# Optimization experiments

Measured on AMD Instinct MI355X. Metric: run time of the kernel, lower is better.

Reference implementation:

```python
import jax, jax.numpy as jnp
import numpy as np

B, C, H, W = 4, 256, 64, 64
RC = 32  # reduced channels = C // reduction


def setup_inputs() -> dict:
    key = jax.random.key(0)
    ks = jax.random.split(key, 5)
    return {
        "x": jax.random.normal(ks[0], (B, C, H, W), dtype=jnp.float32),
        "context": jax.random.normal(ks[1], (B, C, H, W), dtype=jnp.float32),
        "Wq": jax.random.normal(ks[2], (RC, C), dtype=jnp.float32) * 0.02,
        "bq": jnp.zeros((RC,), dtype=jnp.float32),
        "Wk": jax.random.normal(ks[3], (RC, C), dtype=jnp.float32) * 0.02,
        "bk": jnp.zeros((RC,), dtype=jnp.float32),
        "Wv": jax.random.normal(ks[4], (C, C), dtype=jnp.float32) * 0.02,
        "bv": jnp.zeros((C,), dtype=jnp.float32),
        "gamma": jnp.ones((1,), dtype=jnp.float32),
    }


def reference(x, context, Wq, bq, Wk, bk, Wv, bv, gamma):
    b, c, h, w = x.shape
    _, _, hc, wc = context.shape
    n, m = h * w, hc * wc
    xf = x.reshape(b, c, n)          # (B,C,N)
    cf = context.reshape(b, c, m)    # (B,C,M)
    # 1x1 conv projections == per-pixel linear
    q = jnp.einsum('rc,bcn->bnr', Wq, xf) + bq            # (B,N,RC)
    k = jnp.einsum('rc,bcm->brm', Wk, cf) + bk[:, None]   # (B,RC,M)
    v = jnp.einsum('dc,bcm->bdm', Wv, cf) + bv[:, None]   # (B,C,M)
    scale = 1.0 / jnp.sqrt(jnp.asarray(q.shape[-1], dtype=q.dtype))
    attn = jax.nn.softmax(jnp.einsum('bnr,brm->bnm', q, k) * scale, axis=-1)  # (B,N,M)
    out = jnp.einsum('bdm,bnm->bdn', v, attn).reshape(b, c, h, w)
    return gamma * out + x
```

## Files before the change

### kernel.cpp

```cpp
#include <hip/hip_runtime.h>
#include <hip/hip_bf16.h>


#define B_ 4
#define C_ 256
#define N_ 4096
#define M_ 4096
#define SCALE2_ 0.25509558269734695f

typedef __bf16 bf16x8 __attribute__((ext_vector_type(8)));
typedef float f32x4 __attribute__((ext_vector_type(4)));
typedef float f32x16 __attribute__((ext_vector_type(16)));
typedef int i32x8 __attribute__((ext_vector_type(8)));

#define AS1 __attribute__((address_space(1)))
#define AS3 __attribute__((address_space(3)))

static __device__ __forceinline__ unsigned short f2bf(float f) {
    unsigned int u = __float_as_uint(f);
    return (unsigned short)((u + 0x7fffu + ((u >> 16) & 1u)) >> 16);
}
static __device__ __forceinline__ unsigned bfpk(float a, float b) {
    return (unsigned)f2bf(a) | ((unsigned)f2bf(b) << 16);
}
static __device__ __forceinline__ void p_barrier() {
    asm volatile("s_waitcnt lgkmcnt(0)" ::: "memory");
    __builtin_amdgcn_s_barrier();
    asm volatile("" ::: "memory");
}

__global__ __launch_bounds__(256) void prep(
        const float* __restrict__ Wq, const float* __restrict__ Wk,
        const float* __restrict__ Wv, uint4* __restrict__ Wqf,
        uint4* __restrict__ Wkf, uint4* __restrict__ Wvf) {
    int bid = blockIdx.x, t = threadIdx.x;
    const float* W;
    uint4* dst;
    int frag;
    if (bid < 32)      { W = Wv; dst = Wvf; frag = (bid * 256 + t) >> 6; }
    else if (bid < 36) { W = Wq; dst = Wqf; frag = ((bid - 32) * 256 + t) >> 6; }
    else               { W = Wk; dst = Wkf; frag = ((bid - 36) * 256 + t) >> 6; }
    int lane = t & 63, low = lane & 15, q = lane >> 4;
    int fch = frag & 7, fr = frag >> 3;
    const float* wp = W + (size_t)(fr * 16 + low) * C_ + fch * 32 + q * 8;
    float4 w0 = *(const float4*)wp;
    float4 w1 = *(const float4*)(wp + 4);
    uint4 pk = {bfpk(w0.x, w0.y), bfpk(w0.z, w0.w),
                bfpk(w1.x, w1.y), bfpk(w1.z, w1.w)};
    dst[(size_t)frag * 64 + lane] = pk;
}

__global__ __launch_bounds__(256, 2) void fused_proj(
        const float* __restrict__ x, const float* __restrict__ ctx,
        const uint4* __restrict__ Wqf, const uint4* __restrict__ Wkf,
        const uint4* __restrict__ Wvf,
        const float* __restrict__ bq, const float* __restrict__ bk,
        const float* __restrict__ bv,
        unsigned short* __restrict__ Qf, unsigned short* __restrict__ Kf,
        unsigned char* __restrict__ Vf) {
    __shared__ unsigned short X[64][264];
    __shared__ unsigned short Pl[4][16 * 40];
    __shared__ unsigned char  Vw[4][16 * 40];

    int bid = blockIdx.x;
    bool isX = bid >= 256;
    int lb = bid & 255;
    int b = lb >> 6, pt64 = lb & 63;
    const float* __restrict__ in = (isX ? x : ctx) + (size_t)b * C_ * N_ + pt64 * 64;
    int t = threadIdx.x, wg = t >> 6, lane = t & 63;
    int low = lane & 15, q = lane >> 4;

    {
        int pL = lane;
        const float* s0 = in + pL;
#pragma unroll
        for (int ct = 0; ct < 4; ct++) {
            const float* s2 = s0 + (size_t)(ct * 64 + wg * 16) * N_;
            float v[16];
#pragma unroll
            for (int k = 0; k < 16; k++) v[k] = s2[(size_t)k * N_];
#pragma unroll
            for (int k = 0; k < 16; k += 2)
                *(unsigned*)&X[pL][ct * 64 + wg * 16 + k] = bfpk(v[k], v[k + 1]);
        }
    }
    __syncthreads();

    {
        const uint4* __restrict__ Wf = isX ? Wqf : Wkf;
        const float* __restrict__ bias = isX ? bq : bk;
        unsigned short* __restrict__ dst = isX ? Qf : Kf;
        bf16x8 xf[8];
#pragma unroll
        for (int ch = 0; ch < 8; ch++)
            xf[ch] = *(const bf16x8*)&X[wg * 16 + low][ch * 32 + q * 8];
        const f32x4 zero = {0.f, 0.f, 0.f, 0.f};
        f32x4 acc[2] = {zero, zero};
#pragma unroll
        for (int rt = 0; rt < 2; rt++)
#pragma unroll
            for (int ch = 0; ch < 8; ch++) {
                uint4 wv = Wf[(rt * 8 + ch) * 64 + lane];
                acc[rt] = __builtin_amdgcn_mfma_f32_16x16x32_bf16(
                    __builtin_bit_cast(bf16x8, wv), xf[ch], acc[rt], 0, 0, 0);
            }
        unsigned short* Pw = &Pl[wg][0];
#pragma unroll
        for (int rt = 0; rt < 2; rt++) {
            float b0 = bias[rt * 16 + q * 4 + 0], b1 = bias[rt * 16 + q * 4 + 1];
            float b2 = bias[rt * 16 + q * 4 + 2], b3 = bias[rt * 16 + q * 4 + 3];
            uint2 pk = {bfpk(acc[rt][0] + b0, acc[rt][1] + b1),
                        bfpk(acc[rt][2] + b2, acc[rt][3] + b3)};
            *(uint2*)(Pw + low * 40 + rt * 16 + q * 4) = pk;
        }
        uint4 frag = *(const uint4*)(Pw + low * 40 + q * 8);
        ((uint4*)dst)[((size_t)b * 256 + pt64 * 4 + wg) * 64 + lane] = frag;
    }

    if (!isX) {
        int mstep = wg >> 1, dh = wg & 1;
        bf16x8 vfr[2][8];
#pragma unroll
        for (int mt = 0; mt < 2; mt++)
#pragma unroll
            for (int ch = 0; ch < 8; ch++)
                vfr[mt][ch] = *(const bf16x8*)&X[mstep * 32 + mt * 16 + low][ch * 32 + q * 8];
        unsigned char* Vv = &Vw[wg][0];
        int msg = pt64 * 2 + mstep;
        const f32x4 zero = {0.f, 0.f, 0.f, 0.f};
#pragma unroll
        for (int dt8 = 0; dt8 < 8; dt8++) {
            int dt = dh * 8 + dt8;
            f32x4 a0 = zero, a1 = zero;
#pragma unroll
            for (int ch = 0; ch < 8; ch++) {
                uint4 wv = Wvf[(dt * 8 + ch) * 64 + lane];
                bf16x8 wfr = __builtin_bit_cast(bf16x8, wv);
                a0 = __builtin_amdgcn_mfma_f32_16x16x32_bf16(vfr[0][ch], wfr, a0, 0, 0, 0);
                a1 = __builtin_amdgcn_mfma_f32_16x16x32_bf16(vfr[1][ch], wfr, a1, 0, 0, 0);
            }
            float bb = bv[dt * 16 + low];
            unsigned w0 = __builtin_amdgcn_cvt_pk_fp8_f32(a0[0] + bb, a0[1] + bb, 0, false);
            w0 = __builtin_amdgcn_cvt_pk_fp8_f32(a0[2] + bb, a0[3] + bb, w0, true);
            unsigned w1 = __builtin_amdgcn_cvt_pk_fp8_f32(a1[0] + bb, a1[1] + bb, 0, false);
            w1 = __builtin_amdgcn_cvt_pk_fp8_f32(a1[2] + bb, a1[3] + bb, w1, true);
            *(unsigned*)(Vv + low * 40 + q * 4) = w0;
            *(unsigned*)(Vv + low * 40 + 16 + q * 4) = w1;
            uint2 fr = *(const uint2*)(Vv + low * 40 + q * 8);
            ((uint2*)Vf)[(((size_t)b * 128 + msg) * 16 + dt) * 64 + lane] = fr;
        }
    }
}

__global__ __launch_bounds__(256, 4) void attn(
        const unsigned short* __restrict__ Qf, const unsigned short* __restrict__ Kf,
        const unsigned char* __restrict__ Vf, const float* __restrict__ x,
        const float* __restrict__ gamma, float* __restrict__ out) {
    __shared__ __align__(16) unsigned char Pb[2][2560];
    __shared__ float l_sh[2][32];
    __shared__ unsigned Ot[32 * 129];

    int bid = blockIdx.x;
    int xcd = bid & 7;
    int b = xcd >> 1;
    int ng = ((xcd & 1) << 6) | (bid >> 3);

    int wg = threadIdx.x >> 6, lane = threadIdx.x & 63;
    int q = lane >> 4, low = lane & 15;
    int hi = lane >> 5;
    int dsel = q & 1;
    int l31 = lane & 31;
    int t = wg & 1;
    int h = wg >> 1;

    const uint4* Qp = (const uint4*)Qf;
    const uint4* Kp = (const uint4*)Kf + (size_t)b * 256 * 64;
    const uint2* Vq = (const uint2*)(Vf + (size_t)b * 1048576) + (size_t)hi * 1024 + low;

    bf16x8 qa = __builtin_bit_cast(bf16x8, Qp[(size_t)(b * 256 + ng * 2 + t) * 64 + lane]);

    f32x16 acc2[2];
    acc2[0] = (f32x16)(0.f);
    acc2[1] = (f32x16)(0.f);
    float lacc = 0.f;
    const f32x4 zero = {0.f, 0.f, 0.f, 0.f};

    uint4 kv[2];
    f32x4 s[2];
    {
#pragma unroll
        for (int u = 0; u < 2; u++)
            kv[u] = Kp[(size_t)(h * 2 + u) * 64 + lane];
#pragma unroll
        for (int u = 0; u < 2; u++)
            s[u] = __builtin_amdgcn_mfma_f32_16x16x32_bf16(
                __builtin_bit_cast(bf16x8, kv[u]), qa, zero, 0, 0, 0);
#pragma unroll
        for (int u = 0; u < 2; u++)
            kv[u] = Kp[(size_t)(4 + h * 2 + u) * 64 + lane];
        unsigned char* Pw = &Pb[0][0];
#pragma unroll
        for (int u = 0; u < 2; u++) {
            float p0 = __builtin_amdgcn_exp2f(s[u][0] * SCALE2_);
            float p1 = __builtin_amdgcn_exp2f(s[u][1] * SCALE2_);
            float p2 = __builtin_amdgcn_exp2f(s[u][2] * SCALE2_);
            float p3 = __builtin_amdgcn_exp2f(s[u][3] * SCALE2_);
            lacc += p0 + p1 + p2 + p3;
            unsigned w = __builtin_amdgcn_cvt_pk_fp8_f32(p0, p1, 0, false);
            w = __builtin_amdgcn_cvt_pk_fp8_f32(p2, p3, w, true);
            *(unsigned*)(Pw + t * 1280 + low * 80 + h * 32 + u * 16 + q * 4) = w;
        }
    }
    i32x8 vf[2];
#pragma unroll
    for (int dg = 0; dg < 2; dg++) {
        int dt = wg * 4 + dg * 2 + dsel;
        const uint2* Vs = Vq + dt * 64;
        long* dqw = (long*)&vf[dg];
#pragma unroll
        for (int ss = 0; ss < 4; ss++)
            dqw[ss] = *(const long*)(Vs + ss * 16);
    }
    p_barrier();

    for (int i = 0; i < 64; i++) {
        int cur = i & 1, nxt = cur ^ 1;
        bool hn = (i + 1 < 64);

        if (hn) {
#pragma unroll
            for (int u = 0; u < 2; u++)
                s[u] = __builtin_amdgcn_mfma_f32_16x16x32_bf16(
                    __builtin_bit_cast(bf16x8, kv[u]), qa, zero, 0, 0, 0);
            if (i + 2 < 64) {
#pragma unroll
                for (int u = 0; u < 2; u++)
                    kv[u] = Kp[(size_t)((i + 2) * 4 + h * 2 + u) * 64 + lane];
            }
        }

        {
            const unsigned char* pr = &Pb[cur][0] + dsel * 1280 + low * 80 + hi * 32;
            i32x8 pf;
            ((uint4*)&pf)[0] = *(const uint4*)pr;
            ((uint4*)&pf)[1] = *(const uint4*)(pr + 16);
#pragma unroll
            for (int dg = 0; dg < 2; dg++)
                acc2[dg] = __builtin_amdgcn_mfma_scale_f32_32x32x64_f8f6f4(
                    vf[dg], pf, acc2[dg], 0, 0, 0, 127, 0, 127);
        }

        if (hn) {
#pragma unroll
            for (int dg = 0; dg < 2; dg++) {
                int dt = wg * 4 + dg * 2 + dsel;
                const uint2* Vs = Vq + (size_t)(i + 1) * 2048 + dt * 64;
                long* dqw = (long*)&vf[dg];
#pragma unroll
                for (int ss = 0; ss < 4; ss++)
                    dqw[ss] = *(const long*)(Vs + ss * 16);
            }
        }

        if (hn) {
            unsigned char* Pw = &Pb[nxt][0];
#pragma unroll
            for (int u = 0; u < 2; u++) {
                float p0 = __builtin_amdgcn_exp2f(s[u][0] * SCALE2_);
                float p1 = __builtin_amdgcn_exp2f(s[u][1] * SCALE2_);
                float p2 = __builtin_amdgcn_exp2f(s[u][2] * SCALE2_);
                float p3 = __builtin_amdgcn_exp2f(s[u][3] * SCALE2_);
                lacc += p0 + p1 + p2 + p3;
                unsigned w = __builtin_amdgcn_cvt_pk_fp8_f32(p0, p1, 0, false);
                w = __builtin_amdgcn_cvt_pk_fp8_f32(p2, p3, w, true);
                *(unsigned*)(Pw + t * 1280 + low * 80 + h * 32 + u * 16 + q * 4) = w;
            }
        }
        p_barrier();
    }

    lacc += __shfl_xor(lacc, 16, 64);
    lacc += __shfl_xor(lacc, 32, 64);
    if (lane < 16)
        l_sh[h][t * 16 + low] = lacc;

#pragma unroll
    for (int dg = 0; dg < 2; dg++)
#pragma unroll
        for (int k = 0; k < 8; k++) {
            int col16 = wg * 32 + dg * 16 + (k & 1) + 4 * (k >> 1) + 2 * hi;
            Ot[l31 * 129 + col16] = bfpk(acc2[dg][2 * k], acc2[dg][2 * k + 1]);
        }
    __syncthreads();

    {
        float gm = gamma[0];
        float rinv = gm / (l_sh[0][l31] + l_sh[1][l31]);
        int dh = hi;
#pragma unroll
        for (int dq = 0; dq < 2; dq++) {
            size_t nb = ((size_t)(b * 256 + wg * 64 + dq * 32 + dh * 16)) * 4096
                        + (size_t)ng * 32 + l31;
#pragma unroll 4
            for (int j = 0; j < 16; j++) {
                unsigned pk = Ot[l31 * 129 + wg * 32 + dq * 16 + dh * 8 + (j >> 1)];
                unsigned bits = (j & 1) ? (pk & 0xffff0000u) : (pk << 16);
                float o = __uint_as_float(bits);
                size_t idx = nb + (size_t)j * 4096;
                out[idx] = o * rinv + x[idx];
            }
        }
    }
}

extern "C" void kernel_launch(void* const* d_in, const int* in_sizes, int n_in,
                              void* d_out, int out_size, void* d_ws, size_t ws_size,
                              hipStream_t stream) {
    const float* x     = (const float*)d_in[0];
    const float* ctx   = (const float*)d_in[1];
    const float* Wq    = (const float*)d_in[2];
    const float* bq    = (const float*)d_in[3];
    const float* Wk    = (const float*)d_in[4];
    const float* bk    = (const float*)d_in[5];
    const float* Wv    = (const float*)d_in[6];
    const float* bv    = (const float*)d_in[7];
    const float* gamma = (const float*)d_in[8];
    float* out = (float*)d_out;

    unsigned short* Qf = (unsigned short*)d_ws;
    unsigned short* Kf = Qf + (size_t)B_ * N_ * 32;
    unsigned char*  Vf = (unsigned char*)(Kf + (size_t)B_ * M_ * 32);
    uint4* Wqf = (uint4*)(Vf + (size_t)B_ * M_ * C_);
    uint4* Wkf = Wqf + 16 * 64;
    uint4* Wvf = Wkf + 16 * 64;

    prep<<<40, 256, 0, stream>>>(Wq, Wk, Wv, Wqf, Wkf, Wvf);
    fused_proj<<<512, 256, 0, stream>>>(x, ctx, Wqf, Wkf, Wvf, bq, bk, bv, Qf, Kf, Vf);
    attn<<<512, 256, 0, stream>>>(Qf, Kf, Vf, x, gamma, out);
}
```

Measured before the change: 145.0 us.

## Restructure attention to 16-query blocks with 16x16x128 fp8 MFMA and row-major V

Attention blocks now each handle 16 queries instead of 32, so the grid doubles to 1024 blocks. Each wave owns a 64-channel slice of V and loops over 128-key chunks using 16x16x128 scaled fp8 MFMAs instead of 32x32x64. The projection kernel writes V in a plain channel-major transposed layout, and the LDS staging of the output is dropped, so results are written directly from the accumulators. V fragments are prefetched one iteration ahead, and exp2 with a pre-folded scale is replaced by __expf. The aim is more parallelism and a simpler epilogue, at the cost of reloading Q and K per smaller block and less coalesced V stores.

```diff
diff --git a/kernel.cpp b/kernel.cpp
--- a/kernel.cpp
+++ b/kernel.cpp
@@ -6,11 +6,10 @@
 #define C_ 256
 #define N_ 4096
 #define M_ 4096
-#define SCALE2_ 0.25509558269734695f
+#define SCALE_ 0.17677669529663687f
 
 typedef __bf16 bf16x8 __attribute__((ext_vector_type(8)));
 typedef float f32x4 __attribute__((ext_vector_type(4)));
-typedef float f32x16 __attribute__((ext_vector_type(16)));
 typedef int i32x8 __attribute__((ext_vector_type(8)));
 
 #define AS1 __attribute__((address_space(1)))
@@ -57,10 +56,9 @@
         const float* __restrict__ bq, const float* __restrict__ bk,
         const float* __restrict__ bv,
         unsigned short* __restrict__ Qf, unsigned short* __restrict__ Kf,
-        unsigned char* __restrict__ Vf) {
+        unsigned char* __restrict__ Vt) {
     __shared__ unsigned short X[64][264];
     __shared__ unsigned short Pl[4][16 * 40];
-    __shared__ unsigned char  Vw[4][16 * 40];
 
     int bid = blockIdx.x;
     bool isX = bid >= 256;
@@ -125,7 +123,6 @@
 #pragma unroll
             for (int ch = 0; ch < 8; ch++)
                 vfr[mt][ch] = *(const bf16x8*)&X[mstep * 32 + mt * 16 + low][ch * 32 + q * 8];
-        unsigned char* Vv = &Vw[wg][0];
         int msg = pt64 * 2 + mstep;
         const f32x4 zero = {0.f, 0.f, 0.f, 0.f};
 #pragma unroll
@@ -144,137 +141,120 @@
             w0 = __builtin_amdgcn_cvt_pk_fp8_f32(a0[2] + bb, a0[3] + bb, w0, true);
             unsigned w1 = __builtin_amdgcn_cvt_pk_fp8_f32(a1[0] + bb, a1[1] + bb, 0, false);
             w1 = __builtin_amdgcn_cvt_pk_fp8_f32(a1[2] + bb, a1[3] + bb, w1, true);
-            *(unsigned*)(Vv + low * 40 + q * 4) = w0;
-            *(unsigned*)(Vv + low * 40 + 16 + q * 4) = w1;
-            uint2 fr = *(const uint2*)(Vv + low * 40 + q * 8);
-            ((uint2*)Vf)[(((size_t)b * 128 + msg) * 16 + dt) * 64 + lane] = fr;
+            unsigned* vr = (unsigned*)(Vt + ((size_t)(b * 256 + dt * 16 + low)) * 4096
+                                          + msg * 32 + q * 4);
+            vr[0] = w0;
+            vr[4] = w1;
         }
     }
 }
 
 __global__ __launch_bounds__(256, 4) void attn(
         const unsigned short* __restrict__ Qf, const unsigned short* __restrict__ Kf,
-        const unsigned char* __restrict__ Vf, const float* __restrict__ x,
+        const unsigned char* __restrict__ Vt, const float* __restrict__ x,
         const float* __restrict__ gamma, float* __restrict__ out) {
-    __shared__ __align__(16) unsigned char Pb[2][2560];
-    __shared__ float l_sh[2][32];
-    __shared__ unsigned Ot[32 * 129];
+    __shared__ __align__(16) unsigned char Pb[2][64 * 136];
+    __shared__ float l_sh[4][16];
 
     int bid = blockIdx.x;
-    int xcd = bid & 7;
+    int xcd = bid & 7, cu5 = (bid >> 3) & 31, qs = bid >> 8;
     int b = xcd >> 1;
-    int ng = ((xcd & 1) << 6) | (bid >> 3);
+    int g = ((((xcd & 1) << 5) | cu5) << 2) | qs;
 
     int wg = threadIdx.x >> 6, lane = threadIdx.x & 63;
     int q = lane >> 4, low = lane & 15;
-    int hi = lane >> 5;
-    int dsel = q & 1;
-    int l31 = lane & 31;
-    int t = wg & 1;
-    int h = wg >> 1;
 
     const uint4* Qp = (const uint4*)Qf;
     const uint4* Kp = (const uint4*)Kf + (size_t)b * 256 * 64;
-    const uint2* Vq = (const uint2*)(Vf + (size_t)b * 1048576) + (size_t)hi * 1024 + low;
-
-    bf16x8 qa = __builtin_bit_cast(bf16x8, Qp[(size_t)(b * 256 + ng * 2 + t) * 64 + lane]);
-
-    f32x16 acc2[2];
-    acc2[0] = (f32x16)(0.f);
-    acc2[1] = (f32x16)(0.f);
+    const unsigned char* Vrow = Vt + ((size_t)(b * 256 + wg * 64 + low)) * 4096 + q * 32;
+
+    bf16x8 qa = __builtin_bit_cast(bf16x8, Qp[(size_t)(b * 256 + g) * 64 + lane]);
+
+    f32x4 acc[4];
+#pragma unroll
+    for (int dd = 0; dd < 4; dd++) acc[dd] = (f32x4){0.f, 0.f, 0.f, 0.f};
     float lacc = 0.f;
     const f32x4 zero = {0.f, 0.f, 0.f, 0.f};
 
     uint4 kv[2];
     f32x4 s[2];
+#pragma unroll
+    for (int u = 0; u < 2; u++)
+        kv[u] = Kp[(size_t)(wg * 2 + u) * 64 + lane];
+#pragma unroll
+    for (int u = 0; u < 2; u++)
+        s[u] = __builtin_amdgcn_mfma_f32_16x16x32_bf16(
+            __builtin_bit_cast(bf16x8, kv[u]), qa, zero, 0, 0, 0);
+#pragma unroll
+    for (int u = 0; u < 2; u++)
+        kv[u] = Kp[(size_t)(8 + wg * 2 + u) * 64 + lane];
     {
-#pragma unroll
-        for (int u = 0; u < 2; u++)
-            kv[u] = Kp[(size_t)(h * 2 + u) * 64 + lane];
-#pragma unroll
-        for (int u = 0; u < 2; u++)
-            s[u] = __builtin_amdgcn_mfma_f32_16x16x32_bf16(
-                __builtin_bit_cast(bf16x8, kv[u]), qa, zero, 0, 0, 0);
-#pragma unroll
-        for (int u = 0; u < 2; u++)
-            kv[u] = Kp[(size_t)(4 + h * 2 + u) * 64 + lane];
-        unsigned char* Pw = &Pb[0][0];
+        unsigned char* Pw = &Pb[0][0] + (wg * 16 + low) * 136 + q * 4;
 #pragma unroll
         for (int u = 0; u < 2; u++) {
-            float p0 = __builtin_amdgcn_exp2f(s[u][0] * SCALE2_);
-            float p1 = __builtin_amdgcn_exp2f(s[u][1] * SCALE2_);
-            float p2 = __builtin_amdgcn_exp2f(s[u][2] * SCALE2_);
-            float p3 = __builtin_amdgcn_exp2f(s[u][3] * SCALE2_);
+            float p0 = __expf(s[u][0] * SCALE_), p1 = __expf(s[u][1] * SCALE_);
+            float p2 = __expf(s[u][2] * SCALE_), p3 = __expf(s[u][3] * SCALE_);
             lacc += p0 + p1 + p2 + p3;
             unsigned w = __builtin_amdgcn_cvt_pk_fp8_f32(p0, p1, 0, false);
             w = __builtin_amdgcn_cvt_pk_fp8_f32(p2, p3, w, true);
-            *(unsigned*)(Pw + t * 1280 + low * 80 + h * 32 + u * 16 + q * 4) = w;
-        }
-    }
-    i32x8 vf[2];
-#pragma unroll
-    for (int dg = 0; dg < 2; dg++) {
-        int dt = wg * 4 + dg * 2 + dsel;
-        const uint2* Vs = Vq + dt * 64;
-        long* dqw = (long*)&vf[dg];
-#pragma unroll
-        for (int ss = 0; ss < 4; ss++)
-            dqw[ss] = *(const long*)(Vs + ss * 16);
-    }
+            *(unsigned*)(Pw + u * 16) = w;
+        }
+    }
+    i32x8 vf[4];
+#pragma unroll
+    for (int dd = 0; dd < 4; dd++)
+        vf[dd] = *(const i32x8*)(Vrow + (size_t)dd * 65536);
     p_barrier();
 
-    for (int i = 0; i < 64; i++) {
+    for (int i = 0; i < 32; i++) {
         int cur = i & 1, nxt = cur ^ 1;
-        bool hn = (i + 1 < 64);
+        bool hn = (i + 1 < 32);
+
+        i32x8 vfn[4];
+        if (hn) {
+#pragma unroll
+            for (int dd = 0; dd < 4; dd++)
+                vfn[dd] = *(const i32x8*)(Vrow + (size_t)dd * 65536 + (i + 1) * 128);
+        }
 
         if (hn) {
 #pragma unroll
             for (int u = 0; u < 2; u++)
                 s[u] = __builtin_amdgcn_mfma_f32_16x16x32_bf16(
                     __builtin_bit_cast(bf16x8, kv[u]), qa, zero, 0, 0, 0);
-            if (i + 2 < 64) {
+            if (i + 2 < 32) {
 #pragma unroll
                 for (int u = 0; u < 2; u++)
-                    kv[u] = Kp[(size_t)((i + 2) * 4 + h * 2 + u) * 64 + lane];
+                    kv[u] = Kp[(size_t)((i + 2) * 8 + wg * 2 + u) * 64 + lane];
             }
         }
 
         {
-            const unsigned char* pr = &Pb[cur][0] + dsel * 1280 + low * 80 + hi * 32;
+            const unsigned char* pr = &Pb[cur][0] + lane * 136;
             i32x8 pf;
-            ((uint4*)&pf)[0] = *(const uint4*)pr;
-            ((uint4*)&pf)[1] = *(const uint4*)(pr + 16);
-#pragma unroll
-            for (int dg = 0; dg < 2; dg++)
-                acc2[dg] = __builtin_amdgcn_mfma_scale_f32_32x32x64_f8f6f4(
-                    vf[dg], pf, acc2[dg], 0, 0, 0, 127, 0, 127);
+            long* pq = (long*)&pf;
+#pragma unroll
+            for (int j = 0; j < 4; j++)
+                pq[j] = *(const long*)(pr + j * 8);
+#pragma unroll
+            for (int dd = 0; dd < 4; dd++)
+                acc[dd] = __builtin_amdgcn_mfma_scale_f32_16x16x128_f8f6f4(
+                    vf[dd], pf, acc[dd], 0, 0, 0, 127, 0, 127);
         }
 
         if (hn) {
-#pragma unroll
-            for (int dg = 0; dg < 2; dg++) {
-                int dt = wg * 4 + dg * 2 + dsel;
-                const uint2* Vs = Vq + (size_t)(i + 1) * 2048 + dt * 64;
-                long* dqw = (long*)&vf[dg];
-#pragma unroll
-                for (int ss = 0; ss < 4; ss++)
-                    dqw[ss] = *(const long*)(Vs + ss * 16);
-            }
-        }
-
-        if (hn) {
-            unsigned char* Pw = &Pb[nxt][0];
+            unsigned char* Pw = &Pb[nxt][0] + (wg * 16 + low) * 136 + q * 4;
 #pragma unroll
             for (int u = 0; u < 2; u++) {
-                float p0 = __builtin_amdgcn_exp2f(s[u][0] * SCALE2_);
-                float p1 = __builtin_amdgcn_exp2f(s[u][1] * SCALE2_);
-                float p2 = __builtin_amdgcn_exp2f(s[u][2] * SCALE2_);
-                float p3 = __builtin_amdgcn_exp2f(s[u][3] * SCALE2_);
+                float p0 = __expf(s[u][0] * SCALE_), p1 = __expf(s[u][1] * SCALE_);
+                float p2 = __expf(s[u][2] * SCALE_), p3 = __expf(s[u][3] * SCALE_);
                 lacc += p0 + p1 + p2 + p3;
                 unsigned w = __builtin_amdgcn_cvt_pk_fp8_f32(p0, p1, 0, false);
                 w = __builtin_amdgcn_cvt_pk_fp8_f32(p2, p3, w, true);
-                *(unsigned*)(Pw + t * 1280 + low * 80 + h * 32 + u * 16 + q * 4) = w;
-            }
+                *(unsigned*)(Pw + u * 16) = w;
+            }
+#pragma unroll
+            for (int dd = 0; dd < 4; dd++) vf[dd] = vfn[dd];
         }
         p_barrier();
     }
@@ -282,32 +262,20 @@
     lacc += __shfl_xor(lacc, 16, 64);
     lacc += __shfl_xor(lacc, 32, 64);
     if (lane < 16)
-        l_sh[h][t * 16 + low] = lacc;
-
-#pragma unroll
-    for (int dg = 0; dg < 2; dg++)
-#pragma unroll
-        for (int k = 0; k < 8; k++) {
-            int col16 = wg * 32 + dg * 16 + (k & 1) + 4 * (k >> 1) + 2 * hi;
-            Ot[l31 * 129 + col16] = bfpk(acc2[dg][2 * k], acc2[dg][2 * k + 1]);
-        }
+        l_sh[wg][low] = lacc;
     __syncthreads();
 
     {
         float gm = gamma[0];
-        float rinv = gm / (l_sh[0][l31] + l_sh[1][l31]);
-        int dh = hi;
-#pragma unroll
-        for (int dq = 0; dq < 2; dq++) {
-            size_t nb = ((size_t)(b * 256 + wg * 64 + dq * 32 + dh * 16)) * 4096
-                        + (size_t)ng * 32 + l31;
-#pragma unroll 4
-            for (int j = 0; j < 16; j++) {
-                unsigned pk = Ot[l31 * 129 + wg * 32 + dq * 16 + dh * 8 + (j >> 1)];
-                unsigned bits = (j & 1) ? (pk & 0xffff0000u) : (pk << 16);
-                float o = __uint_as_float(bits);
-                size_t idx = nb + (size_t)j * 4096;
-                out[idx] = o * rinv + x[idx];
+        float l = l_sh[0][low] + l_sh[1][low] + l_sh[2][low] + l_sh[3][low];
+        float rinv = gm / l;
+#pragma unroll
+        for (int dd = 0; dd < 4; dd++) {
+            int d = wg * 64 + dd * 16 + q * 4;
+#pragma unroll
+            for (int r = 0; r < 4; r++) {
+                size_t idx = ((size_t)(b * 256 + d + r)) * 4096 + g * 16 + low;
+                out[idx] = acc[dd][r] * rinv + x[idx];
             }
         }
     }
@@ -329,12 +297,12 @@
 
     unsigned short* Qf = (unsigned short*)d_ws;
     unsigned short* Kf = Qf + (size_t)B_ * N_ * 32;
-    unsigned char*  Vf = (unsigned char*)(Kf + (size_t)B_ * M_ * 32);
-    uint4* Wqf = (uint4*)(Vf + (size_t)B_ * M_ * C_);
+    unsigned char*  Vt = (unsigned char*)(Kf + (size_t)B_ * M_ * 32);
+    uint4* Wqf = (uint4*)(Vt + (size_t)B_ * M_ * C_);
     uint4* Wkf = Wqf + 16 * 64;
     uint4* Wvf = Wkf + 16 * 64;
 
     prep<<<40, 256, 0, stream>>>(Wq, Wk, Wv, Wqf, Wkf, Wvf);
-    fused_proj<<<512, 256, 0, stream>>>(x, ctx, Wqf, Wkf, Wvf, bq, bk, bv, Qf, Kf, Vf);
-    attn<<<512, 256, 0, stream>>>(Qf, Kf, Vf, x, gamma, out);
-}
+    fused_proj<<<512, 256, 0, stream>>>(x, ctx, Wqf, Wkf, Wvf, bq, bk, bv, Qf, Kf, Vt);
+    attn<<<1024, 256, 0, stream>>>(Qf, Kf, Vt, x, gamma, out);
+}
```

New measurement: 225.2 us. +55.3%, slower.
